# Performance work log

Measured on AMD Instinct MI355X. Metric: run time of the kernel, lower is better.

## Reference

```python
import jax, jax.numpy as jnp
import numpy as np

B, A, K, M = 8, 100000, 80, 32
ALPHA, GAMMA = 0.25, 2.0


def _make_boxes(rng, n, img=800.0):
    cx = rng.uniform(0, img, n).astype(np.float32)
    cy = rng.uniform(0, img, n).astype(np.float32)
    w = rng.uniform(16, 256, n).astype(np.float32)
    h = rng.uniform(16, 256, n).astype(np.float32)
    return np.stack([cx - w / 2, cy - h / 2, cx + w / 2, cy + h / 2], axis=1)


def setup_inputs() -> dict:
    key = jax.random.key(0)
    k1, k2 = jax.random.split(key)
    rng = np.random.default_rng(0)
    classifications = jax.random.uniform(k1, (B, A, K), dtype=jnp.float32)  # forward clamps to (1e-4, 1-1e-4)
    regressions = jax.random.normal(k2, (B, A, 4), dtype=jnp.float32)
    anchors = jnp.asarray(_make_boxes(rng, A))[None]  # [1, A, 4]
    boxes = _make_boxes(rng, B * M).reshape(B, M, 4)
    labels = rng.integers(0, K, (B, M)).astype(np.float32)
    labels[:, M * 3 // 4:] = -1.0  # padded (invalid) annotations
    annotations = jnp.asarray(np.concatenate([boxes, labels[..., None]], axis=-1))  # [B, M, 5]
    return {"classifications": classifications, "regressions": regressions,
            "anchors": anchors, "annotations": annotations}


def _calc_iou(a, b):
    # a: [A,4] anchors, b: [M,4] gt boxes (xyxy)
    area = (b[:, 2] - b[:, 0]) * (b[:, 3] - b[:, 1])  # [M]
    iw = jnp.clip(jnp.minimum(a[:, 2:3], b[None, :, 2]) - jnp.maximum(a[:, 0:1], b[None, :, 0]), 0)
    ih = jnp.clip(jnp.minimum(a[:, 3:4], b[None, :, 3]) - jnp.maximum(a[:, 1:2], b[None, :, 1]), 0)
    inter = iw * ih  # [A,M]
    ua = ((a[:, 2] - a[:, 0]) * (a[:, 3] - a[:, 1]))[:, None] + area[None] - inter
    return inter / jnp.clip(ua, 1e-8)


def _per_image(classification, regression, anchor, ann):
    label = ann[:, 4]
    valid = label != -1.0
    has_ann = jnp.any(valid)

    iou = _calc_iou(anchor, ann[:, :4])           # [A,M]
    iou = jnp.where(valid[None, :], iou, -1.0)    # mask padded annotations
    iou_max = jnp.max(iou, axis=1)                # [A]
    iou_argmax = jnp.argmax(iou, axis=1)
    assigned = ann[iou_argmax]                    # [A,5]

    positive = iou_max >= 0.5
    num_pos = jnp.sum(positive.astype(jnp.float32))
    one_hot = jax.nn.one_hot(assigned[:, 4].astype(jnp.int32), K, dtype=jnp.float32)  # [A,K]

    targets = jnp.where((iou_max >= 0.4)[:, None], 0.25, -1.0)
    targets = jnp.where(positive[:, None], one_hot, targets)  # 0 for pos anchors, 1 at assigned class

    # focal loss (detectron form)
    logit = jnp.clip(classification, 1e-4, 1.0 - 1e-4)
    p = jax.nn.sigmoid(logit)
    term1 = (1.0 - p) ** GAMMA * jnp.log(p)
    term2 = -(p ** GAMMA) * jnp.where(logit >= 0.0,
                                      logit + jax.nn.softplus(-logit),
                                      jax.nn.softplus(logit))
    cls_loss = -jnp.where(targets != 0.0, ALPHA * term1, (1.0 - ALPHA) * term2)
    cls_total = jnp.sum(cls_loss) / jnp.maximum(num_pos, 0.01)

    aw = anchor[:, 2] - anchor[:, 0]
    ah = anchor[:, 3] - anchor[:, 1]
    acx = anchor[:, 0] + 0.5 * aw
    acy = anchor[:, 1] + 0.5 * ah
    gw = assigned[:, 2] - assigned[:, 0]
    gh = assigned[:, 3] - assigned[:, 1]
    gcx = assigned[:, 0] + 0.5 * gw
    gcy = assigned[:, 1] + 0.5 * gh
    gw = jnp.clip(gw, 1.0)
    gh = jnp.clip(gh, 1.0)
    t = jnp.stack([(gcx - acx) / aw, (gcy - acy) / ah,
                   jnp.log(gw / aw), jnp.log(gh / ah)], axis=1)
    t = t / jnp.array([0.1, 0.1, 0.2, 0.2], dtype=jnp.float32)
    diff = jnp.abs(t - regression)
    sl1 = jnp.where(diff <= 1.0 / 9.0, 0.5 * 9.0 * diff * diff, diff - 0.5 / 9.0)
    reg_sum = jnp.sum(jnp.where(positive[:, None], sl1, 0.0))
    reg_loss = jnp.where(num_pos > 0, reg_sum / jnp.maximum(num_pos * 4.0, 1.0), 0.0)

    cls_total = jnp.where(has_ann, cls_total, 0.0)
    reg_loss = jnp.where(has_ann, reg_loss, 0.0)
    return cls_total, reg_loss


def reference(classifications, regressions, anchors, annotations):
    cls_l, reg_l = jax.vmap(_per_image, in_axes=(0, 0, None, 0))(
        classifications, regressions, anchors[0], annotations)
    return (jnp.mean(cls_l, keepdims=True), jnp.mean(reg_l, keepdims=True))
```

## Files before the change

### kernel.cpp

```cpp
#include <hip/hip_runtime.h>

#define BB 8
#define AA 100000
#define KK 80
#define MM 32
#define NB1 391
#define NB1_P 392
#define K2BLK 256
#define K2STRIDE (K2BLK * 256)
#define TOTAL4 (AA * KK / 4)

__device__ __forceinline__ float cls_term(float c, int code, int k) {
    float x   = __builtin_amdgcn_fmed3f(c, 1e-4f, 1.0f - 1e-4f);
    float em  = __expf(-x);
    float u   = 1.0f + em;
    float s   = __logf(u);
    float p   = __builtin_amdgcn_rcpf(u);
    float omp = 1.0f - p;
    bool use2 = (code >= 0) && (k != code);
    return use2 ? (0.75f * p * p * (x + s)) : (0.25f * omp * omp * s);
}

__device__ __forceinline__ float neg_term(float c) {
    float x   = __builtin_amdgcn_fmed3f(c, 1e-4f, 1.0f - 1e-4f);
    float em  = __expf(-x);
    float u   = 1.0f + em;
    float s   = __logf(u);
    float p   = __builtin_amdgcn_rcpf(u);
    float omp = 1.0f - p;
    return 0.25f * omp * omp * s;
}

__global__ __launch_bounds__(256)
void focal_anchors(const float* __restrict__ reg,
                   const float* __restrict__ anc,
                   const float* __restrict__ ann,
                   int*   __restrict__ codes,
                   float* __restrict__ reg_part_g,
                   int*   __restrict__ np_part)
{
    const int blk = blockIdx.x;
    const int b   = blockIdx.y;
    const int t   = threadIdx.x;
    const int a   = blk * 256 + t;
    const bool act = (a < AA);

    __shared__ float s_ann[MM * 5];
    __shared__ int   s_wnp[4];
    __shared__ float s_wrg[4];

    if (t < MM * 5) s_ann[t] = ann[b * MM * 5 + t];
    __syncthreads();

    int   code     = -1;
    float reg_part = 0.0f;
    int   pos      = 0;
    if (act) {
        const float4 av = ((const float4*)anc)[a];
        const float ax1 = av.x, ay1 = av.y, ax2 = av.z, ay2 = av.w;
        float best = -2.0f;
        int   bidx = 0;
        const float a_area = (ax2 - ax1) * (ay2 - ay1);
        #pragma unroll
        for (int m = 0; m < MM; ++m) {
            float bx1 = s_ann[m * 5 + 0], by1 = s_ann[m * 5 + 1];
            float bx2 = s_ann[m * 5 + 2], by2 = s_ann[m * 5 + 3];
            float lab = s_ann[m * 5 + 4];
            float area  = (bx2 - bx1) * (by2 - by1);
            float iw    = fmaxf(fminf(ax2, bx2) - fmaxf(ax1, bx1), 0.0f);
            float ih    = fmaxf(fminf(ay2, by2) - fmaxf(ay1, by1), 0.0f);
            float inter = iw * ih;
            float ua    = fmaxf(a_area + area - inter, 1e-8f);
            float iou   = inter / ua;
            if (lab == -1.0f) iou = -1.0f;
            if (iou > best) { best = iou; bidx = m; }
        }
        if (best >= 0.5f) {
            pos  = 1;
            code = (int)s_ann[bidx * 5 + 4];
            float gx1 = s_ann[bidx * 5 + 0], gy1 = s_ann[bidx * 5 + 1];
            float gx2 = s_ann[bidx * 5 + 2], gy2 = s_ann[bidx * 5 + 3];
            float aw  = ax2 - ax1,  ah  = ay2 - ay1;
            float acx = ax1 + 0.5f * aw, acy = ay1 + 0.5f * ah;
            float gw  = gx2 - gx1,  gh  = gy2 - gy1;
            float gcx = gx1 + 0.5f * gw, gcy = gy1 + 0.5f * gh;
            gw = fmaxf(gw, 1.0f); gh = fmaxf(gh, 1.0f);
            float tt0 = ((gcx - acx) / aw) / 0.1f;
            float tt1 = ((gcy - acy) / ah) / 0.1f;
            float tt2 = logf(gw / aw) / 0.2f;
            float tt3 = logf(gh / ah) / 0.2f;
            const float4 rv = ((const float4*)reg)[(size_t)b * AA + a];
            float d0 = fabsf(tt0 - rv.x);
            float d1 = fabsf(tt1 - rv.y);
            float d2 = fabsf(tt2 - rv.z);
            float d3 = fabsf(tt3 - rv.w);
            const float th = 1.0f / 9.0f, hb = 0.5f / 9.0f;
            reg_part  = (d0 <= th ? 4.5f * d0 * d0 : d0 - hb)
                      + (d1 <= th ? 4.5f * d1 * d1 : d1 - hb)
                      + (d2 <= th ? 4.5f * d2 * d2 : d2 - hb)
                      + (d3 <= th ? 4.5f * d3 * d3 : d3 - hb);
        }
    }
    if (act) codes[b * AA + a] = code;

    {
        unsigned long long bal = __ballot(pos != 0);
        int wnp = __popcll(bal);
        float wrg = reg_part;
        #pragma unroll
        for (int off = 32; off > 0; off >>= 1) wrg += __shfl_down(wrg, off, 64);
        if ((t & 63) == 0) { s_wnp[t >> 6] = wnp; s_wrg[t >> 6] = wrg; }
    }
    __syncthreads();
    if (t == 0) {
        np_part   [b * NB1_P + blk] = s_wnp[0] + s_wnp[1] + s_wnp[2] + s_wnp[3];
        reg_part_g[b * NB1_P + blk] = s_wrg[0] + s_wrg[1] + s_wrg[2] + s_wrg[3];
    }
}

__global__ __launch_bounds__(256, 8)
void focal_cls(const float* __restrict__ cls,
               const int*   __restrict__ codes,
               float* __restrict__ cls_part)
{
    const int b   = blockIdx.y;
    const int t   = threadIdx.x;
    const int gid = blockIdx.x * 256 + t;
    const float4* __restrict__ c4  = (const float4*)(cls + (size_t)b * ((size_t)AA * KK));
    const int*    __restrict__ cod = codes + b * AA;

    float part = 0.0f;

    auto process = [&](const float4 vv, int g) {
        unsigned q  = (unsigned)g / 20u;
        unsigned k0 = ((unsigned)g - q * 20u) * 4u;
        int ca = cod[q];
        if (__ballot(ca >= 0) == 0ULL) {
            part += neg_term(vv.x);
            part += neg_term(vv.y);
            part += neg_term(vv.z);
            part += neg_term(vv.w);
        } else {
            part += cls_term(vv.x, ca, (int)k0);
            part += cls_term(vv.y, ca, (int)k0 + 1);
            part += cls_term(vv.z, ca, (int)k0 + 2);
            part += cls_term(vv.w, ca, (int)k0 + 3);
        }
    };

    #pragma unroll 1
    for (int sc = 0; sc < 3; ++sc) {
        const int g0 = gid + sc * 8 * K2STRIDE;
        float4 v[8];
        #pragma unroll
        for (int j = 0; j < 8; ++j) v[j] = c4[g0 + j * K2STRIDE];
        #pragma unroll
        for (int j = 0; j < 8; ++j) process(v[j], g0 + j * K2STRIDE);
    }
    {
        const int g0 = gid + 24 * K2STRIDE;
        float4 v[7];
        #pragma unroll
        for (int j = 0; j < 7; ++j) {
            int g = g0 + j * K2STRIDE;
            if (g < TOTAL4) v[j] = c4[g];
        }
        #pragma unroll
        for (int j = 0; j < 7; ++j) {
            int g = g0 + j * K2STRIDE;
            if (g < TOTAL4) process(v[j], g);
        }
    }

    __shared__ float s_wred[4];
    #pragma unroll
    for (int off = 32; off > 0; off >>= 1) part += __shfl_down(part, off, 64);
    if ((t & 63) == 0) s_wred[t >> 6] = part;
    __syncthreads();
    if (t == 0)
        cls_part[b * K2BLK + blockIdx.x] = s_wred[0] + s_wred[1] + s_wred[2] + s_wred[3];
}

__global__ __launch_bounds__(256)
void focal_final(const float* __restrict__ ann,
                 const float* __restrict__ cls_part,
                 const float* __restrict__ reg_part,
                 const int*   __restrict__ np_part,
                 float* __restrict__ out)
{
    const int t    = threadIdx.x;
    const int lane = t & 63, wid = t >> 6;
    __shared__ double sd[4];
    __shared__ float  sf[4];
    __shared__ int    si[4];
    __shared__ float  s_c[BB], s_r[BB];

    for (int b = 0; b < BB; ++b) {
        double cd = (double)cls_part[b * K2BLK + t];
        float rf = 0.0f; int np = 0;
        for (int j = t; j < NB1; j += 256) {
            rf += reg_part[b * NB1_P + j];
            np += np_part [b * NB1_P + j];
        }
        #pragma unroll
        for (int off = 32; off > 0; off >>= 1) {
            cd += __shfl_down(cd, off, 64);
            rf += __shfl_down(rf, off, 64);
            np += __shfl_down(np, off, 64);
        }
        if (lane == 0) { sd[wid] = cd; sf[wid] = rf; si[wid] = np; }
        __syncthreads();
        if (t == 0) {
            double cdt = sd[0] + sd[1] + sd[2] + sd[3];
            float  rft = sf[0] + sf[1] + sf[2] + sf[3];
            int    npt = si[0] + si[1] + si[2] + si[3];
            bool has = false;
            for (int m = 0; m < MM; ++m)
                has |= (ann[b * MM * 5 + m * 5 + 4] != -1.0f);
            float npf  = (float)npt;
            float ctot = (float)cdt / fmaxf(npf, 0.01f);
            float rtot = (npt > 0) ? (rft / fmaxf(npf * 4.0f, 1.0f)) : 0.0f;
            s_c[b] = has ? ctot : 0.0f;
            s_r[b] = has ? rtot : 0.0f;
        }
        __syncthreads();
    }
    if (t == 0) {
        float c = 0.0f, r = 0.0f;
        for (int b = 0; b < BB; ++b) { c += s_c[b]; r += s_r[b]; }
        out[0] = c / (float)BB;
        out[1] = r / (float)BB;
    }
}

extern "C" void kernel_launch(void* const* d_in, const int* in_sizes, int n_in,
                              void* d_out, int out_size, void* d_ws, size_t ws_size,
                              hipStream_t stream) {
    const float* cls = (const float*)d_in[0];
    const float* reg = (const float*)d_in[1];
    const float* anc = (const float*)d_in[2];
    const float* ann = (const float*)d_in[3];
    float* out = (float*)d_out;

    int*   codes    = (int*)d_ws;
    float* cls_part = (float*)(codes + (size_t)BB * AA);
    float* reg_part = cls_part + BB * K2BLK;
    int*   np_part  = (int*)(reg_part + BB * NB1_P);

    dim3 g1(NB1, BB);
    focal_anchors<<<g1, 256, 0, stream>>>(reg, anc, ann, codes, reg_part, np_part);

    dim3 g2(K2BLK, BB);
    focal_cls<<<g2, 256, 0, stream>>>(cls, codes, cls_part);

    focal_final<<<1, 256, 0, stream>>>(ann, cls_part, reg_part, np_part, out);
}
```

Baseline: 399.3 us.

## Split focal loss into dense negative sum plus sparse positive-anchor corrections

Computes the negative-class focal term for every element in a dependency-free kernel and moves the positive-anchor corrections into the anchor kernel, which re-reads only the cls rows of positive anchors. This removes the per-anchor codes buffer, the integer divide and the lookup per float4, and the branchy mixed path. It also changes the unroll depth and occupancy hint of the streaming kernel. The positive-anchor rows are read twice, and summing in a different order slightly changes floating-point rounding.

```diff
diff --git a/kernel.cpp b/kernel.cpp
--- a/kernel.cpp
+++ b/kernel.cpp
@@ -7,19 +7,8 @@
 #define NB1 391
 #define NB1_P 392
 #define K2BLK 256
-#define K2STRIDE (K2BLK * 256)
+#define K2CH  (K2BLK * 256)
 #define TOTAL4 (AA * KK / 4)
-
-__device__ __forceinline__ float cls_term(float c, int code, int k) {
-    float x   = __builtin_amdgcn_fmed3f(c, 1e-4f, 1.0f - 1e-4f);
-    float em  = __expf(-x);
-    float u   = 1.0f + em;
-    float s   = __logf(u);
-    float p   = __builtin_amdgcn_rcpf(u);
-    float omp = 1.0f - p;
-    bool use2 = (code >= 0) && (k != code);
-    return use2 ? (0.75f * p * p * (x + s)) : (0.25f * omp * omp * s);
-}
 
 __device__ __forceinline__ float neg_term(float c) {
     float x   = __builtin_amdgcn_fmed3f(c, 1e-4f, 1.0f - 1e-4f);
@@ -31,11 +20,24 @@
     return 0.25f * omp * omp * s;
 }
 
+__device__ __forceinline__ float corr_term(float c, int ca, int k) {
+    float x   = __builtin_amdgcn_fmed3f(c, 1e-4f, 1.0f - 1e-4f);
+    float em  = __expf(-x);
+    float u   = 1.0f + em;
+    float s   = __logf(u);
+    float p   = __builtin_amdgcn_rcpf(u);
+    float omp = 1.0f - p;
+    float t2  = 0.75f * p * p * (x + s);
+    float t1  = 0.25f * omp * omp * s;
+    return (k == ca) ? 0.0f : (t2 - t1);
+}
+
 __global__ __launch_bounds__(256)
-void focal_anchors(const float* __restrict__ reg,
+void focal_anchors(const float* __restrict__ cls,
+                   const float* __restrict__ reg,
                    const float* __restrict__ anc,
                    const float* __restrict__ ann,
-                   int*   __restrict__ codes,
+                   float* __restrict__ corr_part,
                    float* __restrict__ reg_part_g,
                    int*   __restrict__ np_part)
 {
@@ -48,6 +50,7 @@
     __shared__ float s_ann[MM * 5];
     __shared__ int   s_wnp[4];
     __shared__ float s_wrg[4];
+    __shared__ float s_wcr[4];
 
     if (t < MM * 5) s_ann[t] = ann[b * MM * 5 + t];
     __syncthreads();
@@ -101,74 +104,82 @@
                       + (d3 <= th ? 4.5f * d3 * d3 : d3 - hb);
         }
     }
-    if (act) codes[b * AA + a] = code;
+
+    float corr = 0.0f;
+    {
+        unsigned long long bal = __ballot(pos != 0);
+        const int lane = t & 63;
+        const float* __restrict__ crow_base = cls + (size_t)b * ((size_t)AA * KK);
+        while (bal) {
+            int l = __ffsll((long long)bal) - 1;
+            bal &= bal - 1;
+            int ca   = __shfl(code, l, 64);
+            int aIdx = (blk * 256 + (t & ~63)) + l;
+            const float* crow = crow_base + (size_t)aIdx * KK;
+            float c0 = crow[lane];
+            corr += corr_term(c0, ca, lane);
+            if (lane < 16) {
+                float c1 = crow[64 + lane];
+                corr += corr_term(c1, ca, 64 + lane);
+            }
+        }
+    }
 
     {
         unsigned long long bal = __ballot(pos != 0);
         int wnp = __popcll(bal);
-        float wrg = reg_part;
-        #pragma unroll
-        for (int off = 32; off > 0; off >>= 1) wrg += __shfl_down(wrg, off, 64);
-        if ((t & 63) == 0) { s_wnp[t >> 6] = wnp; s_wrg[t >> 6] = wrg; }
+        float wrg = reg_part, wcr = corr;
+        #pragma unroll
+        for (int off = 32; off > 0; off >>= 1) {
+            wrg += __shfl_down(wrg, off, 64);
+            wcr += __shfl_down(wcr, off, 64);
+        }
+        if ((t & 63) == 0) {
+            s_wnp[t >> 6] = wnp; s_wrg[t >> 6] = wrg; s_wcr[t >> 6] = wcr;
+        }
     }
     __syncthreads();
     if (t == 0) {
         np_part   [b * NB1_P + blk] = s_wnp[0] + s_wnp[1] + s_wnp[2] + s_wnp[3];
         reg_part_g[b * NB1_P + blk] = s_wrg[0] + s_wrg[1] + s_wrg[2] + s_wrg[3];
-    }
-}
-
-__global__ __launch_bounds__(256, 8)
-void focal_cls(const float* __restrict__ cls,
-               const int*   __restrict__ codes,
-               float* __restrict__ cls_part)
+        corr_part [b * NB1_P + blk] = s_wcr[0] + s_wcr[1] + s_wcr[2] + s_wcr[3];
+    }
+}
+
+__global__ __launch_bounds__(256, 6)
+void focal_neg(const float* __restrict__ cls,
+               float* __restrict__ neg_part)
 {
     const int b   = blockIdx.y;
     const int t   = threadIdx.x;
     const int gid = blockIdx.x * 256 + t;
-    const float4* __restrict__ c4  = (const float4*)(cls + (size_t)b * ((size_t)AA * KK));
-    const int*    __restrict__ cod = codes + b * AA;
+    const float4* __restrict__ c4 =
+        (const float4*)(cls + (size_t)b * ((size_t)AA * KK));
 
     float part = 0.0f;
-
-    auto process = [&](const float4 vv, int g) {
-        unsigned q  = (unsigned)g / 20u;
-        unsigned k0 = ((unsigned)g - q * 20u) * 4u;
-        int ca = cod[q];
-        if (__ballot(ca >= 0) == 0ULL) {
-            part += neg_term(vv.x);
-            part += neg_term(vv.y);
-            part += neg_term(vv.z);
-            part += neg_term(vv.w);
-        } else {
-            part += cls_term(vv.x, ca, (int)k0);
-            part += cls_term(vv.y, ca, (int)k0 + 1);
-            part += cls_term(vv.z, ca, (int)k0 + 2);
-            part += cls_term(vv.w, ca, (int)k0 + 3);
-        }
-    };
 
     #pragma unroll 1
     for (int sc = 0; sc < 3; ++sc) {
-        const int g0 = gid + sc * 8 * K2STRIDE;
-        float4 v[8];
-        #pragma unroll
-        for (int j = 0; j < 8; ++j) v[j] = c4[g0 + j * K2STRIDE];
-        #pragma unroll
-        for (int j = 0; j < 8; ++j) process(v[j], g0 + j * K2STRIDE);
+        const int g0 = gid + sc * 10 * K2CH;
+        float4 v[10];
+        #pragma unroll
+        for (int j = 0; j < 10; ++j) v[j] = c4[g0 + j * K2CH];
+        #pragma unroll
+        for (int j = 0; j < 10; ++j) {
+            part += neg_term(v[j].x);
+            part += neg_term(v[j].y);
+            part += neg_term(v[j].z);
+            part += neg_term(v[j].w);
+        }
     }
     {
-        const int g0 = gid + 24 * K2STRIDE;
-        float4 v[7];
-        #pragma unroll
-        for (int j = 0; j < 7; ++j) {
-            int g = g0 + j * K2STRIDE;
-            if (g < TOTAL4) v[j] = c4[g];
-        }
-        #pragma unroll
-        for (int j = 0; j < 7; ++j) {
-            int g = g0 + j * K2STRIDE;
-            if (g < TOTAL4) process(v[j], g);
+        const int g = gid + 30 * K2CH;
+        if (g < TOTAL4) {
+            float4 v = c4[g];
+            part += neg_term(v.x);
+            part += neg_term(v.y);
+            part += neg_term(v.z);
+            part += neg_term(v.w);
         }
     }
 
@@ -178,12 +189,14 @@
     if ((t & 63) == 0) s_wred[t >> 6] = part;
     __syncthreads();
     if (t == 0)
-        cls_part[b * K2BLK + blockIdx.x] = s_wred[0] + s_wred[1] + s_wred[2] + s_wred[3];
+        neg_part[b * K2BLK + blockIdx.x] =
+            s_wred[0] + s_wred[1] + s_wred[2] + s_wred[3];
 }
 
 __global__ __launch_bounds__(256)
 void focal_final(const float* __restrict__ ann,
-                 const float* __restrict__ cls_part,
+                 const float* __restrict__ neg_part,
+                 const float* __restrict__ corr_part,
                  const float* __restrict__ reg_part,
                  const int*   __restrict__ np_part,
                  float* __restrict__ out)
@@ -196,9 +209,10 @@
     __shared__ float  s_c[BB], s_r[BB];
 
     for (int b = 0; b < BB; ++b) {
-        double cd = (double)cls_part[b * K2BLK + t];
+        double cd = (double)neg_part[b * K2BLK + t];
         float rf = 0.0f; int np = 0;
         for (int j = t; j < NB1; j += 256) {
+            cd += (double)corr_part[b * NB1_P + j];
             rf += reg_part[b * NB1_P + j];
             np += np_part [b * NB1_P + j];
         }
@@ -242,16 +256,18 @@
     const float* ann = (const float*)d_in[3];
     float* out = (float*)d_out;
 
-    int*   codes    = (int*)d_ws;
-    float* cls_part = (float*)(codes + (size_t)BB * AA);
-    float* reg_part = cls_part + BB * K2BLK;
-    int*   np_part  = (int*)(reg_part + BB * NB1_P);
+    float* neg_part  = (float*)d_ws;
+    float* corr_part = neg_part + BB * K2BLK;
+    float* reg_part  = corr_part + BB * NB1_P;
+    int*   np_part   = (int*)(reg_part + BB * NB1_P);
+
+    dim3 g2(K2BLK, BB);
+    focal_neg<<<g2, 256, 0, stream>>>(cls, neg_part);
 
     dim3 g1(NB1, BB);
-    focal_anchors<<<g1, 256, 0, stream>>>(reg, anc, ann, codes, reg_part, np_part);
-
-    dim3 g2(K2BLK, BB);
-    focal_cls<<<g2, 256, 0, stream>>>(cls, codes, cls_part);
-
-    focal_final<<<1, 256, 0, stream>>>(ann, cls_part, reg_part, np_part, out);
-}
+    focal_anchors<<<g1, 256, 0, stream>>>(cls, reg, anc, ann,
+                                          corr_part, reg_part, np_part);
+
+    focal_final<<<1, 256, 0, stream>>>(ann, neg_part, corr_part,
+                                       reg_part, np_part, out);
+}
```

After: 404.9 us. About the same (+1.4%).
